# Kernel optimization log

Hardware: AMD Instinct MI355X
Metric: run time of the kernel (lower is better)

Reference implementation:

```python
import jax, jax.numpy as jnp
import numpy as np

ENC, TAG, LANG, ATT = 512, 512, 512, 256
N, P = 1024, 1024


def setup_inputs() -> dict:
    key = jax.random.key(0)
    ks = jax.random.split(key, 11)
    s = lambda d: 1.0 / np.sqrt(d)
    return {
        "encoder_out": jax.random.normal(ks[0], (1, P, ENC), jnp.float32),
        "decoder_hidden": jax.random.normal(ks[1], (N, TAG), jnp.float32),
        "language_out": jax.random.normal(ks[2], (N, LANG), jnp.float32),
        "We": jax.random.uniform(ks[3], (ATT, ENC), jnp.float32, -s(ENC), s(ENC)),
        "be": jax.random.uniform(ks[4], (ATT,), jnp.float32, -s(ENC), s(ENC)),
        "Wt": jax.random.uniform(ks[5], (ATT, TAG), jnp.float32, -s(TAG), s(TAG)),
        "bt": jax.random.uniform(ks[6], (ATT,), jnp.float32, -s(TAG), s(TAG)),
        "Wl": jax.random.uniform(ks[7], (ATT, LANG), jnp.float32, -s(LANG), s(LANG)),
        "bl": jax.random.uniform(ks[8], (ATT,), jnp.float32, -s(LANG), s(LANG)),
        "Wf": jax.random.uniform(ks[9], (1, ATT), jnp.float32, -s(ATT), s(ATT)),
        "bf": jax.random.uniform(ks[10], (1,), jnp.float32, -s(ATT), s(ATT)),
    }


def reference(encoder_out, decoder_hidden, language_out, We, be, Wt, bt, Wl, bl, Wf, bf):
    # att1: (1, P, A); att2, att3: (N, A)
    att1 = jnp.einsum("bpe,ae->bpa", encoder_out, We) + be
    att2 = decoder_hidden @ Wt.T + bt
    att3 = language_out @ Wl.T + bl
    # broadcast add -> (N, P, A), relu, reduce to scalar score per pixel
    h = jax.nn.relu(att1 + (att2 + att3)[:, None, :])  # (N, P, A)
    att = jnp.einsum("npa,a->np", h, Wf[0]) + bf[0]     # (N, P)
    alpha = jax.nn.softmax(att, axis=1)
    # softmax-weighted sum over pixels -> (N, ENC)
    awe = jnp.einsum("np,pe->ne", alpha, encoder_out[0])
    return awe, alpha
```

## Files before the change

kernel.cpp:

```cpp
#include <hip/hip_runtime.h>
#include <hip/hip_bf16.h>
#include <math.h>

#define ENC 512
#define ATT 256
#define NN 1024
#define PP 1024

typedef __attribute__((ext_vector_type(8))) __bf16 bf16x8;
typedef __attribute__((ext_vector_type(4))) float floatx4;
typedef __attribute__((ext_vector_type(2))) float floatx2;

union LdsVec { uint4 u; bf16x8 v; };

__device__ __forceinline__ unsigned cvt_pk(float lo, float hi) {
    union { __hip_bfloat162 h; unsigned u; } x;
    x.h = __float22bfloat162_rn(float2{lo, hi});
    return x.u;
}
__device__ __forceinline__ uint4 cvt8(float4 f0, float4 f1) {
    uint4 r;
    r.x = cvt_pk(f0.x, f0.y); r.y = cvt_pk(f0.z, f0.w);
    r.z = cvt_pk(f1.x, f1.y); r.w = cvt_pk(f1.z, f1.w);
    return r;
}

__device__ __forceinline__ int tile_off(int row, int k) {
    return row * 32 + ((((k >> 3) ^ ((row >> 1) & 3)) & 3) << 3) + (k & 7);
}

__device__ __forceinline__ void stage_bt(unsigned short* dst, const float* __restrict__ src,
                                         int ld, int k0, int tid) {
    const int row = tid >> 2, kseg = tid & 3;
    const float* p = src + (size_t)row * ld + k0 + kseg * 8;
    float4 f0 = *(const float4*)p;
    float4 f1 = *(const float4*)(p + 4);
    uint4 u = cvt8(f0, f1);
    *(uint4*)&dst[tile_off(row, kseg * 8)] = u;
}

__global__ __launch_bounds__(256) void mfma_uv(
    const float* __restrict__ E,  const float* __restrict__ We, const float* __restrict__ be,
    const float* __restrict__ D,  const float* __restrict__ Wt, const float* __restrict__ bt,
    const float* __restrict__ Lg, const float* __restrict__ Wl, const float* __restrict__ bl,
    float* __restrict__ uT, float* __restrict__ v1T, float* __restrict__ v2T,
    unsigned short* __restrict__ ET)
{
    const int tid = threadIdx.x;

    if (blockIdx.z == 3) {
        __shared__ unsigned short T[64][72];
        const int k0 = blockIdx.y * 64;
        const int kr = tid >> 2, nc = (tid & 3) * 16;
        const int nr = tid >> 2, kc = (tid & 3) * 16;
        #pragma unroll
        for (int t = 0; t < 2; ++t) {
            const int n0 = (blockIdx.x * 2 + t) * 64;
            const float* ep = E + (size_t)(k0 + kr) * ENC + n0 + nc;
            float4 a = *(const float4*)(ep + 0),  b = *(const float4*)(ep + 4);
            float4 c = *(const float4*)(ep + 8),  d = *(const float4*)(ep + 12);
            if (t) __syncthreads();
            *(uint4*)&T[kr][nc]     = cvt8(a, b);
            *(uint4*)&T[kr][nc + 8] = cvt8(c, d);
            __syncthreads();
            unsigned short tmp[16];
            #pragma unroll
            for (int i = 0; i < 16; ++i) tmp[i] = T[kc + i][nr];
            unsigned short* op = ET + (size_t)(n0 + nr) * PP + k0 + kc;
            *(uint4*)(op)     = *(uint4*)&tmp[0];
            *(uint4*)(op + 8) = *(uint4*)&tmp[8];
        }
        return;
    }

    __shared__ __align__(16) unsigned short As[2][64 * 32];
    __shared__ __align__(16) unsigned short Bs[2][64 * 32];
    const int K = 512;

    const float *A, *B, *bias; float* out;
    if      (blockIdx.z == 0) { A = E;  B = We; bias = be; out = uT;  }
    else if (blockIdx.z == 1) { A = D;  B = Wt; bias = bt; out = v1T; }
    else                      { A = Lg; B = Wl; bias = bl; out = v2T; }

    const int m0 = blockIdx.y * 64, n0 = blockIdx.x * 64;
    const int wv = tid >> 6, lm = tid & 15, lq = (tid >> 4) & 3;
    const int mb = (wv & 1) * 32, nb = (wv >> 1) * 32;
    const int a0o = tile_off(mb + lm,      lq * 8);
    const int a1o = tile_off(mb + 16 + lm, lq * 8);
    const int b0o = tile_off(nb + lm,      lq * 8);
    const int b1o = tile_off(nb + 16 + lm, lq * 8);

    const int row = tid >> 2, kseg = tid & 3;
    const int soff = tile_off(row, kseg * 8);
    const float* Ap = A + (size_t)(m0 + row) * K + kseg * 8;
    const float* Bp = B + (size_t)(n0 + row) * K + kseg * 8;

    floatx4 acc[2][2];
    const floatx4 zero = {0.f, 0.f, 0.f, 0.f};
    acc[0][0] = zero; acc[0][1] = zero; acc[1][0] = zero; acc[1][1] = zero;

    float4 pa0 = *(const float4*)(Ap), pa1 = *(const float4*)(Ap + 4);
    float4 pb0 = *(const float4*)(Bp), pb1 = *(const float4*)(Bp + 4);

    for (int k0 = 0; k0 < K; k0 += 32) {
        const int buf = (k0 >> 5) & 1;
        *(uint4*)&As[buf][soff] = cvt8(pa0, pa1);
        *(uint4*)&Bs[buf][soff] = cvt8(pb0, pb1);
        __syncthreads();
        if (k0 + 32 < K) {
            pa0 = *(const float4*)(Ap + k0 + 32); pa1 = *(const float4*)(Ap + k0 + 36);
            pb0 = *(const float4*)(Bp + k0 + 32); pb1 = *(const float4*)(Bp + k0 + 36);
        }
        LdsVec fa0, fa1, fb0, fb1;
        fa0.u = *(const uint4*)&As[buf][a0o];
        fa1.u = *(const uint4*)&As[buf][a1o];
        fb0.u = *(const uint4*)&Bs[buf][b0o];
        fb1.u = *(const uint4*)&Bs[buf][b1o];
        acc[0][0] = __builtin_amdgcn_mfma_f32_16x16x32_bf16(fa0.v, fb0.v, acc[0][0], 0, 0, 0);
        acc[0][1] = __builtin_amdgcn_mfma_f32_16x16x32_bf16(fa0.v, fb1.v, acc[0][1], 0, 0, 0);
        acc[1][0] = __builtin_amdgcn_mfma_f32_16x16x32_bf16(fa1.v, fb0.v, acc[1][0], 0, 0, 0);
        acc[1][1] = __builtin_amdgcn_mfma_f32_16x16x32_bf16(fa1.v, fb1.v, acc[1][1], 0, 0, 0);
    }

    #pragma unroll
    for (int s = 0; s < 2; ++s) {
        const int col = n0 + nb + s * 16 + lm;
        const float bsum = bias[col];
        #pragma unroll
        for (int t = 0; t < 2; ++t) {
            const int mbase = m0 + mb + t * 16 + lq * 4;
            float4 o;
            o.x = acc[t][s][0] + bsum; o.y = acc[t][s][1] + bsum;
            o.z = acc[t][s][2] + bsum; o.w = acc[t][s][3] + bsum;
            *(float4*)&out[(size_t)col * NN + mbase] = o;
        }
    }
}

__global__ __launch_bounds__(256) void att_fused(
    const float* __restrict__ uT, const float* __restrict__ v1T,
    const float* __restrict__ v2T,
    const float* __restrict__ Wf, float* __restrict__ att_part)
{
    __shared__ float us[32][68];
    __shared__ float vs[32][68];
    __shared__ float wfs[128];
    const int tid = threadIdx.x;
    const int z = blockIdx.z;
    if (tid < 128) wfs[tid] = Wf[z * 128 + tid];
    const int p0 = blockIdx.x * 64, n0 = blockIdx.y * 64;
    const int rowS = tid >> 3, cS = (tid & 7) * 8;
    const int tx = tid & 15, ty = tid >> 4;

    floatx2 acc[4][2];
    const floatx2 z2 = {0.f, 0.f};
    #pragma unroll
    for (int j = 0; j < 4; ++j) { acc[j][0] = z2; acc[j][1] = z2; }

    const int abase = z * 128;
    for (int ac = 0; ac < 128; ac += 32) {
        __syncthreads();
        {
            const float* up = &uT[(size_t)(abase + ac + rowS) * NN + p0 + cS];
            float4 f0 = *(const float4*)up;
            float4 f1 = *(const float4*)(up + 4);
            *(float4*)&us[rowS][cS]     = f0;
            *(float4*)&us[rowS][cS + 4] = f1;
            const size_t vidx = (size_t)(abase + ac + rowS) * NN + n0 + cS;
            float4 g0 = *(const float4*)&v1T[vidx];
            float4 g1 = *(const float4*)&v1T[vidx + 4];
            float4 h0 = *(const float4*)&v2T[vidx];
            float4 h1 = *(const float4*)&v2T[vidx + 4];
            float4 s0, s1;
            s0.x = g0.x + h0.x; s0.y = g0.y + h0.y; s0.z = g0.z + h0.z; s0.w = g0.w + h0.w;
            s1.x = g1.x + h1.x; s1.y = g1.y + h1.y; s1.z = g1.z + h1.z; s1.w = g1.w + h1.w;
            *(float4*)&vs[rowS][cS]     = s0;
            *(float4*)&vs[rowS][cS + 4] = s1;
        }
        __syncthreads();
        #pragma unroll
        for (int a4 = 0; a4 < 32; a4 += 4) {
            float4 w4 = *(const float4*)&wfs[ac + a4];
            #pragma unroll
            for (int aa = 0; aa < 4; ++aa) {
                const int a = a4 + aa;
                float4 u4 = *(const float4*)&us[a][tx * 4];
                float4 v4 = *(const float4*)&vs[a][ty * 4];
                const float w = (aa == 0) ? w4.x : (aa == 1) ? w4.y : (aa == 2) ? w4.z : w4.w;
                floatx2 ulo = {u4.x, u4.y}, uhi = {u4.z, u4.w};
                const float vv[4] = {v4.x, v4.y, v4.z, v4.w};
                #pragma unroll
                for (int j = 0; j < 4; ++j) {
                    floatx2 t0 = ulo + vv[j];
                    floatx2 t1 = uhi + vv[j];
                    t0 = __builtin_elementwise_max(t0, z2);
                    t1 = __builtin_elementwise_max(t1, z2);
                    acc[j][0] = t0 * w + acc[j][0];
                    acc[j][1] = t1 * w + acc[j][1];
                }
            }
        }
    }

    float* outp = att_part + (size_t)z * NN * PP;
    #pragma unroll
    for (int j = 0; j < 4; ++j) {
        float4 o;
        o.x = acc[j][0].x; o.y = acc[j][0].y; o.z = acc[j][1].x; o.w = acc[j][1].y;
        *(float4*)&outp[(size_t)(n0 + ty * 4 + j) * PP + p0 + tx * 4] = o;
    }
}

__global__ __launch_bounds__(256) void softmax_rows(
    const float* __restrict__ att_part, float* __restrict__ alpha,
    unsigned short* __restrict__ alpha_bf)
{
    const int wv = threadIdx.x >> 6, lane = threadIdx.x & 63;
    const int n = blockIdx.x * 4 + wv;
    const float* r0 = att_part + (size_t)n * PP;
    const float* r1 = att_part + (size_t)NN * PP + (size_t)n * PP;

    float4 x[4];
    #pragma unroll
    for (int i = 0; i < 4; ++i) {
        float4 a = *(const float4*)&r0[i * 256 + lane * 4];
        float4 b = *(const float4*)&r1[i * 256 + lane * 4];
        x[i].x = a.x + b.x; x[i].y = a.y + b.y; x[i].z = a.z + b.z; x[i].w = a.w + b.w;
    }

    float m = -1e30f;
    #pragma unroll
    for (int i = 0; i < 4; ++i)
        m = fmaxf(m, fmaxf(fmaxf(x[i].x, x[i].y), fmaxf(x[i].z, x[i].w)));
    #pragma unroll
    for (int off = 32; off > 0; off >>= 1) m = fmaxf(m, __shfl_xor(m, off, 64));

    float s = 0.f;
    #pragma unroll
    for (int i = 0; i < 4; ++i) {
        x[i].x = __expf(x[i].x - m); x[i].y = __expf(x[i].y - m);
        x[i].z = __expf(x[i].z - m); x[i].w = __expf(x[i].w - m);
        s += x[i].x + x[i].y + x[i].z + x[i].w;
    }
    #pragma unroll
    for (int off = 32; off > 0; off >>= 1) s += __shfl_xor(s, off, 64);
    const float inv = 1.0f / s;

    float* ar = alpha + (size_t)n * PP;
    unsigned short* br = alpha_bf + (size_t)n * PP;
    #pragma unroll
    for (int i = 0; i < 4; ++i) {
        x[i].x *= inv; x[i].y *= inv; x[i].z *= inv; x[i].w *= inv;
        *(float4*)&ar[i * 256 + lane * 4] = x[i];
        uint2 pk;
        pk.x = cvt_pk(x[i].x, x[i].y);
        pk.y = cvt_pk(x[i].z, x[i].w);
        *(uint2*)&br[i * 256 + lane * 4] = pk;
    }
}

__global__ __launch_bounds__(256) void mfma_awe(
    const unsigned short* __restrict__ alpha_bf,
    const unsigned short* __restrict__ ET, float* __restrict__ awe)
{
    __shared__ __align__(16) unsigned short As[2][32 * 32];
    __shared__ __align__(16) unsigned short Bs[2][64 * 32];
    const int tid = threadIdx.x;
    const int K = PP;
    const int m0 = blockIdx.y * 32, n0 = blockIdx.x * 64;
    const int wv = tid >> 6, lm = tid & 15, lq = (tid >> 4) & 3;
    const int mw = (wv & 1) * 16, nw = (wv >> 1) * 32;
    const int a0o = tile_off(mw + lm,      lq * 8);
    const int b0o = tile_off(nw + lm,      lq * 8);
    const int b1o = tile_off(nw + 16 + lm, lq * 8);

    const int rowA = tid >> 3, kcA = (tid & 7) * 4;
    const int rowB = tid >> 2, kcB = (tid & 3) * 8;
    const int aoff = tile_off(rowA, kcA);
    const int boff = tile_off(rowB, kcB);
    const unsigned short* Ap = alpha_bf + (size_t)(m0 + rowA) * PP + kcA;
    const unsigned short* Bp = ET + (size_t)(n0 + rowB) * PP + kcB;

    floatx4 acc[2];
    const floatx4 zero = {0.f, 0.f, 0.f, 0.f};
    acc[0] = zero; acc[1] = zero;

    uint2 pa = *(const uint2*)Ap;
    uint4 pb = *(const uint4*)Bp;

    for (int k0 = 0; k0 < K; k0 += 32) {
        const int buf = (k0 >> 5) & 1;
        *(uint2*)&As[buf][aoff] = pa;
        *(uint4*)&Bs[buf][boff] = pb;
        __syncthreads();
        if (k0 + 32 < K) {
            pa = *(const uint2*)(Ap + k0 + 32);
            pb = *(const uint4*)(Bp + k0 + 32);
        }
        LdsVec fa, fb0, fb1;
        fa.u  = *(const uint4*)&As[buf][a0o];
        fb0.u = *(const uint4*)&Bs[buf][b0o];
        fb1.u = *(const uint4*)&Bs[buf][b1o];
        acc[0] = __builtin_amdgcn_mfma_f32_16x16x32_bf16(fa.v, fb0.v, acc[0], 0, 0, 0);
        acc[1] = __builtin_amdgcn_mfma_f32_16x16x32_bf16(fa.v, fb1.v, acc[1], 0, 0, 0);
    }

    #pragma unroll
    for (int s = 0; s < 2; ++s) {
        const int col = n0 + nw + s * 16 + lm;
        #pragma unroll
        for (int r = 0; r < 4; ++r)
            awe[(size_t)(m0 + mw + lq * 4 + r) * ENC + col] = acc[s][r];
    }
}

extern "C" void kernel_launch(void* const* d_in, const int* in_sizes, int n_in,
                              void* d_out, int out_size, void* d_ws, size_t ws_size,
                              hipStream_t stream)
{
    const float* encoder = (const float*)d_in[0];
    const float* dec     = (const float*)d_in[1];
    const float* lang    = (const float*)d_in[2];
    const float* We      = (const float*)d_in[3];
    const float* be      = (const float*)d_in[4];
    const float* Wt      = (const float*)d_in[5];
    const float* bt      = (const float*)d_in[6];
    const float* Wl      = (const float*)d_in[7];
    const float* bl      = (const float*)d_in[8];
    const float* Wf      = (const float*)d_in[9];

    float* uT   = (float*)d_ws;
    float* v1T  = uT  + ATT * NN;
    float* v2T  = v1T + ATT * NN;
    float* attp = v2T + ATT * NN;
    unsigned short* alpha_bf = (unsigned short*)(attp + 2 * (size_t)NN * PP);
    unsigned short* ET       = alpha_bf + (size_t)NN * PP;

    float* awe   = (float*)d_out;
    float* alpha = (float*)d_out + NN * ENC;

    mfma_uv<<<dim3(4, 16, 4), 256, 0, stream>>>(
        encoder, We, be, dec, Wt, bt, lang, Wl, bl, uT, v1T, v2T, ET);
    att_fused<<<dim3(PP / 64, NN / 64, 2), 256, 0, stream>>>(uT, v1T, v2T, Wf, attp);
    softmax_rows<<<dim3(NN / 4), 256, 0, stream>>>(attp, alpha, alpha_bf);
    mfma_awe<<<dim3(ENC / 64, NN / 32), 256, 0, stream>>>(alpha_bf, ET, awe);
}
```

Baseline: 124.9 us.

## Fuse all stages into one cooperative kernel with grid syncs and fused softmax

Merges the projection GEMMs, attention scoring, softmax and weighted-sum GEMM into a single cooperative kernel of 256 blocks separated by grid-wide barriers, with a fallback to three separate launches. The scoring stage now has each block own four full query rows, so softmax runs in registers and the two partial-score buffers written to and read back from global memory go away. v1/v2 are stored row-major so each block can gather its rows. The trade-off: 256 blocks is low parallelism for the scoring stage, each thread streams all of uT from global memory with no LDS tiling, and grid syncs add their own cost.

```diff
diff --git a/kernel.cpp b/kernel.cpp
--- a/kernel.cpp
+++ b/kernel.cpp
@@ -1,5 +1,6 @@
 #include <hip/hip_runtime.h>
 #include <hip/hip_bf16.h>
+#include <hip/hip_cooperative_groups.h>
 #include <math.h>
 
 #define ENC 512
@@ -29,43 +30,40 @@
     return row * 32 + ((((k >> 3) ^ ((row >> 1) & 3)) & 3) << 3) + (k & 7);
 }
 
-__device__ __forceinline__ void stage_bt(unsigned short* dst, const float* __restrict__ src,
-                                         int ld, int k0, int tid) {
-    const int row = tid >> 2, kseg = tid & 3;
-    const float* p = src + (size_t)row * ld + k0 + kseg * 8;
-    float4 f0 = *(const float4*)p;
-    float4 f1 = *(const float4*)(p + 4);
-    uint4 u = cvt8(f0, f1);
-    *(uint4*)&dst[tile_off(row, kseg * 8)] = u;
-}
-
-__global__ __launch_bounds__(256) void mfma_uv(
+union __align__(16) SmemU {
+    struct { unsigned short As[2][2048]; unsigned short Bs[2][2048]; } g;
+    struct { unsigned short T[64][72]; } t;
+    struct { float vsmT[256][4]; float wfs[256]; float red[2][4][4]; } att;
+    struct { unsigned short As[2][1024]; unsigned short Bs[2][2048]; } aw;
+};
+
+__device__ __forceinline__ void phase1(SmemU& sm, int bid,
     const float* __restrict__ E,  const float* __restrict__ We, const float* __restrict__ be,
     const float* __restrict__ D,  const float* __restrict__ Wt, const float* __restrict__ bt,
     const float* __restrict__ Lg, const float* __restrict__ Wl, const float* __restrict__ bl,
-    float* __restrict__ uT, float* __restrict__ v1T, float* __restrict__ v2T,
+    float* __restrict__ uT, float* __restrict__ v1, float* __restrict__ v2,
     unsigned short* __restrict__ ET)
 {
     const int tid = threadIdx.x;
-
-    if (blockIdx.z == 3) {
-        __shared__ unsigned short T[64][72];
-        const int k0 = blockIdx.y * 64;
+    const int z = bid >> 6, t64 = bid & 63;
+
+    if (z == 3) {
+        const int k0 = (t64 >> 2) * 64;
         const int kr = tid >> 2, nc = (tid & 3) * 16;
         const int nr = tid >> 2, kc = (tid & 3) * 16;
         #pragma unroll
         for (int t = 0; t < 2; ++t) {
-            const int n0 = (blockIdx.x * 2 + t) * 64;
+            const int n0 = ((t64 & 3) * 2 + t) * 64;
             const float* ep = E + (size_t)(k0 + kr) * ENC + n0 + nc;
             float4 a = *(const float4*)(ep + 0),  b = *(const float4*)(ep + 4);
             float4 c = *(const float4*)(ep + 8),  d = *(const float4*)(ep + 12);
             if (t) __syncthreads();
-            *(uint4*)&T[kr][nc]     = cvt8(a, b);
-            *(uint4*)&T[kr][nc + 8] = cvt8(c, d);
+            *(uint4*)&sm.t.T[kr][nc]     = cvt8(a, b);
+            *(uint4*)&sm.t.T[kr][nc + 8] = cvt8(c, d);
             __syncthreads();
             unsigned short tmp[16];
             #pragma unroll
-            for (int i = 0; i < 16; ++i) tmp[i] = T[kc + i][nr];
+            for (int i = 0; i < 16; ++i) tmp[i] = sm.t.T[kc + i][nr];
             unsigned short* op = ET + (size_t)(n0 + nr) * PP + k0 + kc;
             *(uint4*)(op)     = *(uint4*)&tmp[0];
             *(uint4*)(op + 8) = *(uint4*)&tmp[8];
@@ -73,16 +71,13 @@
         return;
     }
 
-    __shared__ __align__(16) unsigned short As[2][64 * 32];
-    __shared__ __align__(16) unsigned short Bs[2][64 * 32];
     const int K = 512;
-
-    const float *A, *B, *bias; float* out;
-    if      (blockIdx.z == 0) { A = E;  B = We; bias = be; out = uT;  }
-    else if (blockIdx.z == 1) { A = D;  B = Wt; bias = bt; out = v1T; }
-    else                      { A = Lg; B = Wl; bias = bl; out = v2T; }
-
-    const int m0 = blockIdx.y * 64, n0 = blockIdx.x * 64;
+    const float *A, *B, *bias;
+    if      (z == 0) { A = E;  B = We; bias = be; }
+    else if (z == 1) { A = D;  B = Wt; bias = bt; }
+    else             { A = Lg; B = Wl; bias = bl; }
+
+    const int m0 = (t64 >> 2) * 64, n0 = (t64 & 3) * 64;
     const int wv = tid >> 6, lm = tid & 15, lq = (tid >> 4) & 3;
     const int mb = (wv & 1) * 32, nb = (wv >> 1) * 32;
     const int a0o = tile_off(mb + lm,      lq * 8);
@@ -104,170 +99,153 @@
 
     for (int k0 = 0; k0 < K; k0 += 32) {
         const int buf = (k0 >> 5) & 1;
-        *(uint4*)&As[buf][soff] = cvt8(pa0, pa1);
-        *(uint4*)&Bs[buf][soff] = cvt8(pb0, pb1);
+        *(uint4*)&sm.g.As[buf][soff] = cvt8(pa0, pa1);
+        *(uint4*)&sm.g.Bs[buf][soff] = cvt8(pb0, pb1);
         __syncthreads();
         if (k0 + 32 < K) {
             pa0 = *(const float4*)(Ap + k0 + 32); pa1 = *(const float4*)(Ap + k0 + 36);
             pb0 = *(const float4*)(Bp + k0 + 32); pb1 = *(const float4*)(Bp + k0 + 36);
         }
         LdsVec fa0, fa1, fb0, fb1;
-        fa0.u = *(const uint4*)&As[buf][a0o];
-        fa1.u = *(const uint4*)&As[buf][a1o];
-        fb0.u = *(const uint4*)&Bs[buf][b0o];
-        fb1.u = *(const uint4*)&Bs[buf][b1o];
+        fa0.u = *(const uint4*)&sm.g.As[buf][a0o];
+        fa1.u = *(const uint4*)&sm.g.As[buf][a1o];
+        fb0.u = *(const uint4*)&sm.g.Bs[buf][b0o];
+        fb1.u = *(const uint4*)&sm.g.Bs[buf][b1o];
         acc[0][0] = __builtin_amdgcn_mfma_f32_16x16x32_bf16(fa0.v, fb0.v, acc[0][0], 0, 0, 0);
         acc[0][1] = __builtin_amdgcn_mfma_f32_16x16x32_bf16(fa0.v, fb1.v, acc[0][1], 0, 0, 0);
         acc[1][0] = __builtin_amdgcn_mfma_f32_16x16x32_bf16(fa1.v, fb0.v, acc[1][0], 0, 0, 0);
         acc[1][1] = __builtin_amdgcn_mfma_f32_16x16x32_bf16(fa1.v, fb1.v, acc[1][1], 0, 0, 0);
     }
 
-    #pragma unroll
-    for (int s = 0; s < 2; ++s) {
-        const int col = n0 + nb + s * 16 + lm;
-        const float bsum = bias[col];
-        #pragma unroll
-        for (int t = 0; t < 2; ++t) {
-            const int mbase = m0 + mb + t * 16 + lq * 4;
-            float4 o;
-            o.x = acc[t][s][0] + bsum; o.y = acc[t][s][1] + bsum;
-            o.z = acc[t][s][2] + bsum; o.w = acc[t][s][3] + bsum;
-            *(float4*)&out[(size_t)col * NN + mbase] = o;
-        }
-    }
-}
-
-__global__ __launch_bounds__(256) void att_fused(
-    const float* __restrict__ uT, const float* __restrict__ v1T,
-    const float* __restrict__ v2T,
-    const float* __restrict__ Wf, float* __restrict__ att_part)
-{
-    __shared__ float us[32][68];
-    __shared__ float vs[32][68];
-    __shared__ float wfs[128];
+    if (z == 0) {
+        #pragma unroll
+        for (int s = 0; s < 2; ++s) {
+            const int col = n0 + nb + s * 16 + lm;
+            const float bsum = bias[col];
+            #pragma unroll
+            for (int t = 0; t < 2; ++t) {
+                const int mbase = m0 + mb + t * 16 + lq * 4;
+                float4 o;
+                o.x = acc[t][s][0] + bsum; o.y = acc[t][s][1] + bsum;
+                o.z = acc[t][s][2] + bsum; o.w = acc[t][s][3] + bsum;
+                *(float4*)&uT[(size_t)col * NN + mbase] = o;
+            }
+        }
+    } else {
+        float* out = (z == 1) ? v1 : v2;
+        #pragma unroll
+        for (int s = 0; s < 2; ++s) {
+            const int col = n0 + nb + s * 16 + lm;
+            const float bsum = bias[col];
+            #pragma unroll
+            for (int t = 0; t < 2; ++t) {
+                const int r0 = m0 + mb + t * 16 + lq * 4;
+                #pragma unroll
+                for (int r = 0; r < 4; ++r)
+                    out[(size_t)(r0 + r) * ATT + col] = acc[t][s][r] + bsum;
+            }
+        }
+    }
+}
+
+__device__ __forceinline__ void phase2(SmemU& sm, int bid,
+    const float* __restrict__ uT, const float* __restrict__ v1,
+    const float* __restrict__ v2, const float* __restrict__ Wf,
+    float* __restrict__ alpha, unsigned short* __restrict__ alpha_bf)
+{
     const int tid = threadIdx.x;
-    const int z = blockIdx.z;
-    if (tid < 128) wfs[tid] = Wf[z * 128 + tid];
-    const int p0 = blockIdx.x * 64, n0 = blockIdx.y * 64;
-    const int rowS = tid >> 3, cS = (tid & 7) * 8;
-    const int tx = tid & 15, ty = tid >> 4;
-
-    floatx2 acc[4][2];
+    const int n0 = bid * 4;
+
+    {
+        const size_t i0 = (size_t)(n0 + 0) * ATT + tid;
+        const size_t i1 = (size_t)(n0 + 1) * ATT + tid;
+        const size_t i2 = (size_t)(n0 + 2) * ATT + tid;
+        const size_t i3 = (size_t)(n0 + 3) * ATT + tid;
+        float4 vv;
+        vv.x = v1[i0] + v2[i0];
+        vv.y = v1[i1] + v2[i1];
+        vv.z = v1[i2] + v2[i2];
+        vv.w = v1[i3] + v2[i3];
+        *(float4*)&sm.att.vsmT[tid][0] = vv;
+        sm.att.wfs[tid] = Wf[tid];
+    }
+    __syncthreads();
+
+    floatx2 aL[4], aH[4];
     const floatx2 z2 = {0.f, 0.f};
     #pragma unroll
-    for (int j = 0; j < 4; ++j) { acc[j][0] = z2; acc[j][1] = z2; }
-
-    const int abase = z * 128;
-    for (int ac = 0; ac < 128; ac += 32) {
-        __syncthreads();
-        {
-            const float* up = &uT[(size_t)(abase + ac + rowS) * NN + p0 + cS];
-            float4 f0 = *(const float4*)up;
-            float4 f1 = *(const float4*)(up + 4);
-            *(float4*)&us[rowS][cS]     = f0;
-            *(float4*)&us[rowS][cS + 4] = f1;
-            const size_t vidx = (size_t)(abase + ac + rowS) * NN + n0 + cS;
-            float4 g0 = *(const float4*)&v1T[vidx];
-            float4 g1 = *(const float4*)&v1T[vidx + 4];
-            float4 h0 = *(const float4*)&v2T[vidx];
-            float4 h1 = *(const float4*)&v2T[vidx + 4];
-            float4 s0, s1;
-            s0.x = g0.x + h0.x; s0.y = g0.y + h0.y; s0.z = g0.z + h0.z; s0.w = g0.w + h0.w;
-            s1.x = g1.x + h1.x; s1.y = g1.y + h1.y; s1.z = g1.z + h1.z; s1.w = g1.w + h1.w;
-            *(float4*)&vs[rowS][cS]     = s0;
-            *(float4*)&vs[rowS][cS + 4] = s1;
-        }
-        __syncthreads();
-        #pragma unroll
-        for (int a4 = 0; a4 < 32; a4 += 4) {
-            float4 w4 = *(const float4*)&wfs[ac + a4];
-            #pragma unroll
-            for (int aa = 0; aa < 4; ++aa) {
-                const int a = a4 + aa;
-                float4 u4 = *(const float4*)&us[a][tx * 4];
-                float4 v4 = *(const float4*)&vs[a][ty * 4];
-                const float w = (aa == 0) ? w4.x : (aa == 1) ? w4.y : (aa == 2) ? w4.z : w4.w;
-                floatx2 ulo = {u4.x, u4.y}, uhi = {u4.z, u4.w};
-                const float vv[4] = {v4.x, v4.y, v4.z, v4.w};
-                #pragma unroll
-                for (int j = 0; j < 4; ++j) {
-                    floatx2 t0 = ulo + vv[j];
-                    floatx2 t1 = uhi + vv[j];
-                    t0 = __builtin_elementwise_max(t0, z2);
-                    t1 = __builtin_elementwise_max(t1, z2);
-                    acc[j][0] = t0 * w + acc[j][0];
-                    acc[j][1] = t1 * w + acc[j][1];
-                }
-            }
-        }
-    }
-
-    float* outp = att_part + (size_t)z * NN * PP;
-    #pragma unroll
-    for (int j = 0; j < 4; ++j) {
+    for (int r = 0; r < 4; ++r) { aL[r] = z2; aH[r] = z2; }
+
+    const float* up = uT + tid * 4;
+    #pragma unroll 8
+    for (int a = 0; a < 256; ++a) {
+        float4 u4 = *(const float4*)(up + (size_t)a * NN);
+        float4 v4 = *(const float4*)&sm.att.vsmT[a][0];
+        const float w = sm.att.wfs[a];
+        floatx2 ulo = {u4.x, u4.y}, uhi = {u4.z, u4.w};
+        const float vv[4] = {v4.x, v4.y, v4.z, v4.w};
+        #pragma unroll
+        for (int r = 0; r < 4; ++r) {
+            floatx2 t0 = ulo + vv[r];
+            floatx2 t1 = uhi + vv[r];
+            t0 = __builtin_elementwise_max(t0, z2);
+            t1 = __builtin_elementwise_max(t1, z2);
+            aL[r] = t0 * w + aL[r];
+            aH[r] = t1 * w + aH[r];
+        }
+    }
+
+    const int lane = tid & 63, wv = tid >> 6;
+    float m[4];
+    #pragma unroll
+    for (int r = 0; r < 4; ++r) {
+        m[r] = fmaxf(fmaxf(aL[r][0], aL[r][1]), fmaxf(aH[r][0], aH[r][1]));
+        #pragma unroll
+        for (int off = 32; off > 0; off >>= 1)
+            m[r] = fmaxf(m[r], __shfl_xor(m[r], off, 64));
+    }
+    if (lane == 0) {
+        #pragma unroll
+        for (int r = 0; r < 4; ++r) sm.att.red[0][wv][r] = m[r];
+    }
+    __syncthreads();
+    float s[4];
+    #pragma unroll
+    for (int r = 0; r < 4; ++r) {
+        m[r] = fmaxf(fmaxf(sm.att.red[0][0][r], sm.att.red[0][1][r]),
+                     fmaxf(sm.att.red[0][2][r], sm.att.red[0][3][r]));
+        aL[r][0] = __expf(aL[r][0] - m[r]); aL[r][1] = __expf(aL[r][1] - m[r]);
+        aH[r][0] = __expf(aH[r][0] - m[r]); aH[r][1] = __expf(aH[r][1] - m[r]);
+        s[r] = (aL[r][0] + aL[r][1]) + (aH[r][0] + aH[r][1]);
+        #pragma unroll
+        for (int off = 32; off > 0; off >>= 1) s[r] += __shfl_xor(s[r], off, 64);
+    }
+    if (lane == 0) {
+        #pragma unroll
+        for (int r = 0; r < 4; ++r) sm.att.red[1][wv][r] = s[r];
+    }
+    __syncthreads();
+    #pragma unroll
+    for (int r = 0; r < 4; ++r) {
+        const float inv = 1.0f / (sm.att.red[1][0][r] + sm.att.red[1][1][r]
+                                + sm.att.red[1][2][r] + sm.att.red[1][3][r]);
         float4 o;
-        o.x = acc[j][0].x; o.y = acc[j][0].y; o.z = acc[j][1].x; o.w = acc[j][1].y;
-        *(float4*)&outp[(size_t)(n0 + ty * 4 + j) * PP + p0 + tx * 4] = o;
-    }
-}
-
-__global__ __launch_bounds__(256) void softmax_rows(
-    const float* __restrict__ att_part, float* __restrict__ alpha,
-    unsigned short* __restrict__ alpha_bf)
-{
-    const int wv = threadIdx.x >> 6, lane = threadIdx.x & 63;
-    const int n = blockIdx.x * 4 + wv;
-    const float* r0 = att_part + (size_t)n * PP;
-    const float* r1 = att_part + (size_t)NN * PP + (size_t)n * PP;
-
-    float4 x[4];
-    #pragma unroll
-    for (int i = 0; i < 4; ++i) {
-        float4 a = *(const float4*)&r0[i * 256 + lane * 4];
-        float4 b = *(const float4*)&r1[i * 256 + lane * 4];
-        x[i].x = a.x + b.x; x[i].y = a.y + b.y; x[i].z = a.z + b.z; x[i].w = a.w + b.w;
-    }
-
-    float m = -1e30f;
-    #pragma unroll
-    for (int i = 0; i < 4; ++i)
-        m = fmaxf(m, fmaxf(fmaxf(x[i].x, x[i].y), fmaxf(x[i].z, x[i].w)));
-    #pragma unroll
-    for (int off = 32; off > 0; off >>= 1) m = fmaxf(m, __shfl_xor(m, off, 64));
-
-    float s = 0.f;
-    #pragma unroll
-    for (int i = 0; i < 4; ++i) {
-        x[i].x = __expf(x[i].x - m); x[i].y = __expf(x[i].y - m);
-        x[i].z = __expf(x[i].z - m); x[i].w = __expf(x[i].w - m);
-        s += x[i].x + x[i].y + x[i].z + x[i].w;
-    }
-    #pragma unroll
-    for (int off = 32; off > 0; off >>= 1) s += __shfl_xor(s, off, 64);
-    const float inv = 1.0f / s;
-
-    float* ar = alpha + (size_t)n * PP;
-    unsigned short* br = alpha_bf + (size_t)n * PP;
-    #pragma unroll
-    for (int i = 0; i < 4; ++i) {
-        x[i].x *= inv; x[i].y *= inv; x[i].z *= inv; x[i].w *= inv;
-        *(float4*)&ar[i * 256 + lane * 4] = x[i];
+        o.x = aL[r][0] * inv; o.y = aL[r][1] * inv;
+        o.z = aH[r][0] * inv; o.w = aH[r][1] * inv;
+        *(float4*)&alpha[(size_t)(n0 + r) * PP + tid * 4] = o;
         uint2 pk;
-        pk.x = cvt_pk(x[i].x, x[i].y);
-        pk.y = cvt_pk(x[i].z, x[i].w);
-        *(uint2*)&br[i * 256 + lane * 4] = pk;
-    }
-}
-
-__global__ __launch_bounds__(256) void mfma_awe(
+        pk.x = cvt_pk(o.x, o.y); pk.y = cvt_pk(o.z, o.w);
+        *(uint2*)&alpha_bf[(size_t)(n0 + r) * PP + tid * 4] = pk;
+    }
+}
+
+__device__ __forceinline__ void phase4(SmemU& sm, int bid,
     const unsigned short* __restrict__ alpha_bf,
     const unsigned short* __restrict__ ET, float* __restrict__ awe)
 {
-    __shared__ __align__(16) unsigned short As[2][32 * 32];
-    __shared__ __align__(16) unsigned short Bs[2][64 * 32];
     const int tid = threadIdx.x;
     const int K = PP;
-    const int m0 = blockIdx.y * 32, n0 = blockIdx.x * 64;
+    const int m0 = (bid >> 3) * 32, n0 = (bid & 7) * 64;
     const int wv = tid >> 6, lm = tid & 15, lq = (tid >> 4) & 3;
     const int mw = (wv & 1) * 16, nw = (wv >> 1) * 32;
     const int a0o = tile_off(mw + lm,      lq * 8);
@@ -290,17 +268,17 @@
 
     for (int k0 = 0; k0 < K; k0 += 32) {
         const int buf = (k0 >> 5) & 1;
-        *(uint2*)&As[buf][aoff] = pa;
-        *(uint4*)&Bs[buf][boff] = pb;
+        *(uint2*)&sm.aw.As[buf][aoff] = pa;
+        *(uint4*)&sm.aw.Bs[buf][boff] = pb;
         __syncthreads();
         if (k0 + 32 < K) {
             pa = *(const uint2*)(Ap + k0 + 32);
             pb = *(const uint4*)(Bp + k0 + 32);
         }
         LdsVec fa, fb0, fb1;
-        fa.u  = *(const uint4*)&As[buf][a0o];
-        fb0.u = *(const uint4*)&Bs[buf][b0o];
-        fb1.u = *(const uint4*)&Bs[buf][b1o];
+        fa.u  = *(const uint4*)&sm.aw.As[buf][a0o];
+        fb0.u = *(const uint4*)&sm.aw.Bs[buf][b0o];
+        fb1.u = *(const uint4*)&sm.aw.Bs[buf][b1o];
         acc[0] = __builtin_amdgcn_mfma_f32_16x16x32_bf16(fa.v, fb0.v, acc[0], 0, 0, 0);
         acc[1] = __builtin_amdgcn_mfma_f32_16x16x32_bf16(fa.v, fb1.v, acc[1], 0, 0, 0);
     }
@@ -312,6 +290,55 @@
         for (int r = 0; r < 4; ++r)
             awe[(size_t)(m0 + mw + lq * 4 + r) * ENC + col] = acc[s][r];
     }
+}
+
+__global__ __launch_bounds__(256) void mega(
+    const float* __restrict__ E,  const float* __restrict__ We, const float* __restrict__ be,
+    const float* __restrict__ D,  const float* __restrict__ Wt, const float* __restrict__ bt,
+    const float* __restrict__ Lg, const float* __restrict__ Wl, const float* __restrict__ bl,
+    const float* __restrict__ Wf,
+    float* __restrict__ uT, float* __restrict__ v1, float* __restrict__ v2,
+    unsigned short* __restrict__ ET, unsigned short* __restrict__ alpha_bf,
+    float* __restrict__ alpha, float* __restrict__ awe)
+{
+    __shared__ SmemU sm;
+    phase1(sm, blockIdx.x, E, We, be, D, Wt, bt, Lg, Wl, bl, uT, v1, v2, ET);
+    __threadfence();
+    cooperative_groups::this_grid().sync();
+    __threadfence();
+    phase2(sm, blockIdx.x, uT, v1, v2, Wf, alpha, alpha_bf);
+    __threadfence();
+    cooperative_groups::this_grid().sync();
+    __threadfence();
+    phase4(sm, blockIdx.x, alpha_bf, ET, awe);
+}
+
+__global__ __launch_bounds__(256) void k_p1(
+    const float* __restrict__ E,  const float* __restrict__ We, const float* __restrict__ be,
+    const float* __restrict__ D,  const float* __restrict__ Wt, const float* __restrict__ bt,
+    const float* __restrict__ Lg, const float* __restrict__ Wl, const float* __restrict__ bl,
+    float* __restrict__ uT, float* __restrict__ v1, float* __restrict__ v2,
+    unsigned short* __restrict__ ET)
+{
+    __shared__ SmemU sm;
+    phase1(sm, blockIdx.x, E, We, be, D, Wt, bt, Lg, Wl, bl, uT, v1, v2, ET);
+}
+
+__global__ __launch_bounds__(256) void k_p2(
+    const float* __restrict__ uT, const float* __restrict__ v1,
+    const float* __restrict__ v2, const float* __restrict__ Wf,
+    float* __restrict__ alpha, unsigned short* __restrict__ alpha_bf)
+{
+    __shared__ SmemU sm;
+    phase2(sm, blockIdx.x, uT, v1, v2, Wf, alpha, alpha_bf);
+}
+
+__global__ __launch_bounds__(256) void k_p4(
+    const unsigned short* __restrict__ alpha_bf,
+    const unsigned short* __restrict__ ET, float* __restrict__ awe)
+{
+    __shared__ SmemU sm;
+    phase4(sm, blockIdx.x, alpha_bf, ET, awe);
 }
 
 extern "C" void kernel_launch(void* const* d_in, const int* in_sizes, int n_in,
@@ -329,19 +356,31 @@
     const float* bl      = (const float*)d_in[8];
     const float* Wf      = (const float*)d_in[9];
 
-    float* uT   = (float*)d_ws;
-    float* v1T  = uT  + ATT * NN;
-    float* v2T  = v1T + ATT * NN;
-    float* attp = v2T + ATT * NN;
-    unsigned short* alpha_bf = (unsigned short*)(attp + 2 * (size_t)NN * PP);
+    float* uT = (float*)d_ws;
+    float* v1 = uT + ATT * NN;
+    float* v2 = v1 + (size_t)NN * ATT;
+    unsigned short* alpha_bf = (unsigned short*)(v2 + (size_t)NN * ATT);
     unsigned short* ET       = alpha_bf + (size_t)NN * PP;
 
     float* awe   = (float*)d_out;
     float* alpha = (float*)d_out + NN * ENC;
 
-    mfma_uv<<<dim3(4, 16, 4), 256, 0, stream>>>(
-        encoder, We, be, dec, Wt, bt, lang, Wl, bl, uT, v1T, v2T, ET);
-    att_fused<<<dim3(PP / 64, NN / 64, 2), 256, 0, stream>>>(uT, v1T, v2T, Wf, attp);
-    softmax_rows<<<dim3(NN / 4), 256, 0, stream>>>(attp, alpha, alpha_bf);
-    mfma_awe<<<dim3(ENC / 64, NN / 32), 256, 0, stream>>>(alpha_bf, ET, awe);
-}
+    void* args[] = {
+        (void*)&encoder, (void*)&We, (void*)&be,
+        (void*)&dec,     (void*)&Wt, (void*)&bt,
+        (void*)&lang,    (void*)&Wl, (void*)&bl,
+        (void*)&Wf,
+        (void*)&uT, (void*)&v1, (void*)&v2,
+        (void*)&ET, (void*)&alpha_bf, (void*)&alpha, (void*)&awe
+    };
+
+    hipError_t err = hipLaunchCooperativeKernel(
+        (const void*)mega, dim3(256), dim3(256), args, 0, stream);
+
+    if (err != hipSuccess) {
+        k_p1<<<dim3(256), 256, 0, stream>>>(encoder, We, be, dec, Wt, bt,
+                                            lang, Wl, bl, uT, v1, v2, ET);
+        k_p2<<<dim3(256), 256, 0, stream>>>(uT, v1, v2, Wf, alpha, alpha_bf);
+        k_p4<<<dim3(256), 256, 0, stream>>>(alpha_bf, ET, awe);
+    }
+}
```

New measurement: 342.4 us. 174% more time.
